# Kernel tuning notes

Hardware: AMD Instinct MI355X
Metric: run time of the kernel (lower is better)

The kernel has to match this reference:

```python
import jax
import jax.numpy as jnp
import numpy as np

# Periodic-boundary copy indices on the padded 18x18 lattice (dst <- src).
# None of the sources is an earlier destination, so one batched gather/scatter is faithful.
DST_R = np.array([1,1,2,3,4,4,6,7,8,10,11,12,14,14,15,16,17,17,16,15,14,14,12,10,8,6,4,4,3,2])
DST_C = np.array([3,5,7,9,10,11,13,13,14,15,15,16,15,16,15,14,13,11,9,7,6,5,3,2,1,0,0,1,1,2])
SRC_R = np.array([13,13,14,15,16,16,6,7,8,10,11,12,2,2,3,4,5,5,4,3,2,2,12,10,8,6,16,16,15,14])
SRC_C = np.array([15,5,7,9,10,11,1,1,2,3,3,4,3,4,3,2,1,11,9,7,6,5,15,14,13,12,12,13,13,14])

# 4x4 kernel sparsity masks (5 taps each)
_UP = np.zeros((4,4), np.float32);    _UP[[0,0,1,2,2],[0,1,1,1,2]] = 1
_LEFT = np.zeros((4,4), np.float32);  _LEFT[[1,2,2,2,3],[1,0,1,2,1]] = 1
_RIGHT = np.zeros((4,4), np.float32); _RIGHT[[1,2,2,2,3],[1,1,2,3,3]] = 1

def _out_mask():
    m = np.ones((16,16), np.float32)
    for i in range(9):
        m[i, 7+i:16] = 0
    for i in range(7):
        m[9+i, 0:i+1] = 0
    m[0,4:7]=0; m[1,6:8]=0; m[2,8]=0; m[3,9]=0
    m[6,12]=0; m[7,13]=0; m[8,14]=0; m[9,14]=0; m[10,14]=0; m[11,15]=0
    m[13:,14:]=0; m[15,13]=0; m[15,7:9]=0; m[13,5]=0; m[14,6]=0
    m[8,0]=0; m[9,1]=0; m[7,0]=0; m[3,0]=0; m[0:3,0:2]=0; m[0,2]=0
    return m
OUT_MASK = _out_mask()

def _conv(x, w, b):
    # kernel 4, stride 2, no padding: [B,C,18,18] -> [B,O,8,8]
    y = jax.lax.conv_general_dilated(x, w, window_strides=(2,2), padding='VALID',
                                     dimension_numbers=('NCHW','OIHW','NCHW'))
    return y + b[None, :, None, None]

def setup_inputs() -> dict:
    key = jax.random.key(0)
    ks = jax.random.split(key, 7)
    B, C, O = 2048, 64, 64
    x = jax.random.normal(ks[0], (B, C, 16, 16), dtype=jnp.float32)
    w_up = jax.random.normal(ks[1], (O, C, 4, 4), dtype=jnp.float32) * 0.05
    b_up = jax.random.normal(ks[2], (O,), dtype=jnp.float32) * 0.05
    w_left = jax.random.normal(ks[3], (O, C, 4, 4), dtype=jnp.float32) * 0.05
    b_left = jax.random.normal(ks[4], (O,), dtype=jnp.float32) * 0.05
    w_right = jax.random.normal(ks[5], (O, C, 4, 4), dtype=jnp.float32) * 0.05
    b_right = jax.random.normal(ks[6], (O,), dtype=jnp.float32) * 0.05
    return {"x": x, "w_up": w_up, "b_up": b_up, "w_left": w_left,
            "b_left": b_left, "w_right": w_right, "b_right": b_right}

def reference(x, w_up, b_up, w_left, b_left, w_right, b_right):
    # 1) zero-pad to 18x18 and apply periodic-boundary indexed copies
    xp = jnp.pad(x, ((0,0),(0,0),(1,1),(1,1)))
    xp = xp.at[:, :, DST_R, DST_C].set(xp[:, :, SRC_R, SRC_C])
    # 2) masked directional convs [B,O,8,8]
    up = _conv(xp, w_up * jnp.asarray(_UP), b_up)
    left = _conv(xp, w_left * jnp.asarray(_LEFT), b_left)
    right = _conv(xp, w_right * jnp.asarray(_RIGHT), b_right)
    # 3) interleave into 16x16: even rows = (up | 0) interleaved cols,
    #    odd rows = (left | right) interleaved cols
    B, O = up.shape[0], up.shape[1]
    out = jnp.zeros((B, O, 16, 16), x.dtype)
    out = out.at[:, :, 0::2, 0::2].set(up)
    out = out.at[:, :, 1::2, 0::2].set(left)
    out = out.at[:, :, 1::2, 1::2].set(right)
    # 4) static zero-out of non-lattice sites
    return out * jnp.asarray(OUT_MASK)
```

## Files before the change

### kernel.cpp

```cpp
#include <hip/hip_runtime.h>
#include <stdint.h>
#include <stddef.h>

typedef __attribute__((ext_vector_type(4))) float    f32x4;
typedef __attribute__((ext_vector_type(2))) float    f32x2;
typedef __attribute__((ext_vector_type(4))) uint32_t u32x4;
typedef __attribute__((ext_vector_type(8))) __bf16   bf16x8;

#define CGS   5200
#define NFRAG 15360

__device__ __constant__ uint8_t TAPR[15] = {0,0,1,2,2, 1,2,2,2,3, 1,2,2,2,3};
__device__ __constant__ uint8_t TAPC[15] = {0,1,1,1,2, 1,0,1,2,1, 1,1,2,3,3};

__device__ __constant__ uint8_t PDR[30] = {1,1,2,3,4,4,6,7,8,10,11,12,14,14,15,16,17,17,16,15,14,14,12,10,8,6,4,4,3,2};
__device__ __constant__ uint8_t PDC[30] = {3,5,7,9,10,11,13,13,14,15,15,16,15,16,15,14,13,11,9,7,6,5,3,2,1,0,0,1,1,2};
__device__ __constant__ uint8_t PSR[30] = {13,13,14,15,16,16,6,7,8,10,11,12,2,2,3,4,5,5,4,3,2,2,12,10,8,6,16,16,15,14};
__device__ __constant__ uint8_t PSC[30] = {15,5,7,9,10,11,1,1,2,3,3,4,3,4,3,2,1,11,9,7,6,5,15,14,13,12,12,13,13,14};

__device__ __forceinline__ uint32_t pk2(float a, float b) {
    return (uint32_t)__builtin_bit_cast(uint16_t, (__bf16)a)
         | ((uint32_t)__builtin_bit_cast(uint16_t, (__bf16)b) << 16);
}

__global__ __launch_bounds__(256) void pack_w(const float* __restrict__ wu,
                                              const float* __restrict__ wl,
                                              const float* __restrict__ wr,
                                              uint16_t* __restrict__ pw) {
    int fid = blockIdx.x * 256 + threadIdx.x;
    if (fid >= NFRAG) return;
    int lane = fid & 63;
    int mt   = (fid >> 6) & 3;
    int kk   = (fid >> 8) & 1;
    int td   = fid >> 9;
    const float* w = (td < 5) ? wu : (td < 10) ? wl : wr;
    int o  = mt * 16 + (lane & 15);
    int cb = kk * 32 + (lane >> 4) * 8;
    int kr = TAPR[td], kc = TAPC[td];
    const float* src = w + ((size_t)o * 64 + cb) * 16 + kr * 4 + kc;
    uint32_t d[4];
#pragma unroll
    for (int p = 0; p < 4; ++p)
        d[p] = pk2(src[(2 * p) * 16], src[(2 * p + 1) * 16]);
    u32x4 v = {d[0], d[1], d[2], d[3]};
    *(u32x4*)(pw + (size_t)fid * 8) = v;
}

__device__ __forceinline__ int slotof(int r, int c) { return (c & 1) * 162 + r * 9 + (c >> 1); }

__global__ __launch_bounds__(256, 3) void kagome_main(const float* __restrict__ x,
                                                      const uint16_t* __restrict__ pw,
                                                      const float* __restrict__ bu,
                                                      const float* __restrict__ bl,
                                                      const float* __restrict__ br,
                                                      float* __restrict__ out) {
    __shared__ __align__(16) uint8_t lds[8 * CGS];
    const int tid = threadIdx.x;
    const int b   = blockIdx.x;

    {
        const float* xb = x + (size_t)b * 16384;
#pragma unroll
        for (int i = 0; i < 2; ++i) {
            const int t    = i * 256 + tid;
            const int cg   = t >> 6;
            const int quad = t & 63;
            const int r0   = quad >> 2;
            const int qc   = quad & 3;
            f32x4 v[8];
#pragma unroll
            for (int ch = 0; ch < 8; ++ch)
                v[ch] = *(const f32x4*)(xb + (cg * 8 + ch) * 256 + quad * 4);
            uint8_t* base = lds + cg * CGS;
#pragma unroll
            for (int e = 0; e < 4; ++e) {
                const int pc   = 4 * qc + e + 1;
                const int slot = slotof(r0 + 1, pc);
                u32x4 w = {pk2(v[0][e], v[1][e]), pk2(v[2][e], v[3][e]),
                           pk2(v[4][e], v[5][e]), pk2(v[6][e], v[7][e])};
                *(u32x4*)(base + slot * 16) = w;
            }
        }
        u32x4 z = {0, 0, 0, 0};
        for (int idx = tid; idx < 68 * 8; idx += 256) {
            int s = idx >> 3, cg = idx & 7;
            int r, c;
            if (s < 18)      { r = 0;  c = s; }
            else if (s < 36) { r = 17; c = s - 18; }
            else             { int k2 = s - 36; r = 1 + (k2 >> 1); c = (k2 & 1) * 17; }
            *(u32x4*)(lds + cg * CGS + slotof(r, c) * 16) = z;
        }
    }
    __syncthreads();
    if (tid < 240) {
        int pair = tid >> 3, cg = tid & 7;
        int sa = slotof(PSR[pair], PSC[pair]);
        int da = slotof(PDR[pair], PDC[pair]);
        u32x4 v = *(const u32x4*)(lds + cg * CGS + sa * 16);
        *(u32x4*)(lds + cg * CGS + da * 16) = v;
    }
    __syncthreads();

    const int l   = tid & 63;
    const int wid = tid >> 6;
    const int q   = l >> 4;
    const int io  = (l >> 3) & 1;
    const int j   = l & 7;

    f32x4 acc[3][4];
#pragma unroll
    for (int d2 = 0; d2 < 3; ++d2)
#pragma unroll
        for (int n2 = 0; n2 < 4; ++n2) acc[d2][n2] = (f32x4){0.f, 0.f, 0.f, 0.f};

    const int bbase = q * CGS + io * 288 + j * 16;
    const uint16_t* pwl = pw + (size_t)l * 8;

#pragma unroll
    for (int kk = 0; kk < 2; ++kk) {
        bf16x8 aw[15];
#pragma unroll
        for (int f2 = 0; f2 < 15; ++f2) {
            u32x4 t = *(const u32x4*)(pwl + (size_t)((f2 * 2 + kk) * 4 + wid) * 512);
            aw[f2] = __builtin_bit_cast(bf16x8, t);
        }
        const uint8_t* lb = lds + kk * (4 * CGS) + bbase;
#pragma unroll
        for (int nt = 0; nt < 4; ++nt) {
#define BRD(dr, dc) __builtin_bit_cast(bf16x8, *(const u32x4*)(lb + ((dc) & 1) * 2592 + (4 * nt + (dr)) * 144 + ((dc) >> 1) * 16))
            bf16x8 b00 = BRD(0, 0);
            acc[0][nt] = __builtin_amdgcn_mfma_f32_16x16x32_bf16(aw[0], b00, acc[0][nt], 0, 0, 0);
            bf16x8 b01 = BRD(0, 1);
            acc[0][nt] = __builtin_amdgcn_mfma_f32_16x16x32_bf16(aw[1], b01, acc[0][nt], 0, 0, 0);
            bf16x8 b11 = BRD(1, 1);
            acc[0][nt] = __builtin_amdgcn_mfma_f32_16x16x32_bf16(aw[2],  b11, acc[0][nt], 0, 0, 0);
            acc[1][nt] = __builtin_amdgcn_mfma_f32_16x16x32_bf16(aw[5],  b11, acc[1][nt], 0, 0, 0);
            acc[2][nt] = __builtin_amdgcn_mfma_f32_16x16x32_bf16(aw[10], b11, acc[2][nt], 0, 0, 0);
            bf16x8 b20 = BRD(2, 0);
            acc[1][nt] = __builtin_amdgcn_mfma_f32_16x16x32_bf16(aw[6],  b20, acc[1][nt], 0, 0, 0);
            bf16x8 b21 = BRD(2, 1);
            acc[0][nt] = __builtin_amdgcn_mfma_f32_16x16x32_bf16(aw[3],  b21, acc[0][nt], 0, 0, 0);
            acc[1][nt] = __builtin_amdgcn_mfma_f32_16x16x32_bf16(aw[7],  b21, acc[1][nt], 0, 0, 0);
            acc[2][nt] = __builtin_amdgcn_mfma_f32_16x16x32_bf16(aw[11], b21, acc[2][nt], 0, 0, 0);
            bf16x8 b22 = BRD(2, 2);
            acc[0][nt] = __builtin_amdgcn_mfma_f32_16x16x32_bf16(aw[4],  b22, acc[0][nt], 0, 0, 0);
            acc[1][nt] = __builtin_amdgcn_mfma_f32_16x16x32_bf16(aw[8],  b22, acc[1][nt], 0, 0, 0);
            acc[2][nt] = __builtin_amdgcn_mfma_f32_16x16x32_bf16(aw[12], b22, acc[2][nt], 0, 0, 0);
            bf16x8 b23 = BRD(2, 3);
            acc[2][nt] = __builtin_amdgcn_mfma_f32_16x16x32_bf16(aw[13], b23, acc[2][nt], 0, 0, 0);
            bf16x8 b31 = BRD(3, 1);
            acc[1][nt] = __builtin_amdgcn_mfma_f32_16x16x32_bf16(aw[9],  b31, acc[1][nt], 0, 0, 0);
            bf16x8 b33 = BRD(3, 3);
            acc[2][nt] = __builtin_amdgcn_mfma_f32_16x16x32_bf16(aw[14], b33, acc[2][nt], 0, 0, 0);
#undef BRD
        }
    }

    float bias0[4], bias1[4], bias2[4];
#pragma unroll
    for (int r = 0; r < 4; ++r) {
        int o = wid * 16 + q * 4 + r;
        bias0[r] = bu[o]; bias1[r] = bl[o]; bias2[r] = br[o];
    }

    constexpr uint32_t RM[16] = {0x0008, 0x003C, 0x00FC, 0x01FE, 0x07FF, 0x0FFF, 0x0FFF, 0x1FFE,
                                 0x3FFE, 0xBFFC, 0xBFFC, 0x7FF8, 0xFFF0, 0x3FC0, 0x3F80, 0x1E00};
#pragma unroll
    for (int nt = 0; nt < 4; ++nt) {
        const int row_e = 4 * nt + 2 * io;
        const uint32_t me = io ? RM[4 * nt + 2] : RM[4 * nt + 0];
        const uint32_t mo = io ? RM[4 * nt + 3] : RM[4 * nt + 1];
        const uint32_t be  = (me >> (2 * j)) & 1u;
        const uint32_t bo0 = (mo >> (2 * j)) & 1u;
        const uint32_t bo1 = (mo >> (2 * j + 1)) & 1u;
#pragma unroll
        for (int r = 0; r < 4; ++r) {
            int o = wid * 16 + q * 4 + r;
            float up = acc[0][nt][r] + bias0[r];
            float lf = acc[1][nt][r] + bias1[r];
            float rt = acc[2][nt][r] + bias2[r];
            up = be  ? up : 0.f;
            lf = bo0 ? lf : 0.f;
            rt = bo1 ? rt : 0.f;
            float* po = out + (((size_t)b * 64 + o) * 256 + row_e * 16 + 2 * j);
            *(f32x2*)po        = (f32x2){up, 0.f};
            *(f32x2*)(po + 16) = (f32x2){lf, rt};
        }
    }
}

extern "C" void kernel_launch(void* const* d_in, const int* in_sizes, int n_in,
                              void* d_out, int out_size, void* d_ws, size_t ws_size,
                              hipStream_t stream) {
    const float* x  = (const float*)d_in[0];
    const float* wu = (const float*)d_in[1];
    const float* bu = (const float*)d_in[2];
    const float* wl = (const float*)d_in[3];
    const float* bl = (const float*)d_in[4];
    const float* wr = (const float*)d_in[5];
    const float* br = (const float*)d_in[6];
    float* out   = (float*)d_out;
    uint16_t* pw = (uint16_t*)d_ws;

    int B = in_sizes[0] / 16384;
    pack_w<<<(NFRAG + 255) / 256, 256, 0, stream>>>(wu, wl, wr, pw);
    kagome_main<<<B, 256, 0, stream>>>(x, pw, bu, bl, br, out);
}
```

Measured before the change: 62.44 us.

## Split each image's N tiles across 8 waves with 512-thread blocks

Doubles the block to 512 threads so each wave computes two of the four spatial N-tiles instead of all four, halving per-wave accumulators and MFMA work. The input staging loop collapses to one iteration per thread. The aim is more latency hiding and shorter per-block critical paths. In exchange, each wave pair reloads the same A-fragment weights from global memory, doubling weight traffic, and the launch-bounds occupancy target of 6 may constrain register allocation.

After: 86.78 us. +39.0%, slower.

```diff
diff --git a/kernel.cpp b/kernel.cpp
--- a/kernel.cpp
+++ b/kernel.cpp
@@ -48,7 +48,7 @@
 
 __device__ __forceinline__ int slotof(int r, int c) { return (c & 1) * 162 + r * 9 + (c >> 1); }
 
-__global__ __launch_bounds__(256, 3) void kagome_main(const float* __restrict__ x,
+__global__ __launch_bounds__(512, 6) void kagome_main(const float* __restrict__ x,
                                                       const uint16_t* __restrict__ pw,
                                                       const float* __restrict__ bu,
                                                       const float* __restrict__ bl,
@@ -60,35 +60,31 @@
 
     {
         const float* xb = x + (size_t)b * 16384;
-#pragma unroll
-        for (int i = 0; i < 2; ++i) {
-            const int t    = i * 256 + tid;
-            const int cg   = t >> 6;
-            const int quad = t & 63;
-            const int r0   = quad >> 2;
-            const int qc   = quad & 3;
-            f32x4 v[8];
-#pragma unroll
-            for (int ch = 0; ch < 8; ++ch)
-                v[ch] = *(const f32x4*)(xb + (cg * 8 + ch) * 256 + quad * 4);
-            uint8_t* base = lds + cg * CGS;
-#pragma unroll
-            for (int e = 0; e < 4; ++e) {
-                const int pc   = 4 * qc + e + 1;
-                const int slot = slotof(r0 + 1, pc);
-                u32x4 w = {pk2(v[0][e], v[1][e]), pk2(v[2][e], v[3][e]),
-                           pk2(v[4][e], v[5][e]), pk2(v[6][e], v[7][e])};
-                *(u32x4*)(base + slot * 16) = w;
-            }
+        const int cg   = tid >> 6;
+        const int quad = tid & 63;
+        const int r0   = quad >> 2;
+        const int qc   = quad & 3;
+        f32x4 v[8];
+#pragma unroll
+        for (int ch = 0; ch < 8; ++ch)
+            v[ch] = *(const f32x4*)(xb + (cg * 8 + ch) * 256 + quad * 4);
+        uint8_t* base = lds + cg * CGS;
+#pragma unroll
+        for (int e = 0; e < 4; ++e) {
+            const int pc   = 4 * qc + e + 1;
+            const int slot = slotof(r0 + 1, pc);
+            u32x4 w = {pk2(v[0][e], v[1][e]), pk2(v[2][e], v[3][e]),
+                       pk2(v[4][e], v[5][e]), pk2(v[6][e], v[7][e])};
+            *(u32x4*)(base + slot * 16) = w;
         }
         u32x4 z = {0, 0, 0, 0};
-        for (int idx = tid; idx < 68 * 8; idx += 256) {
-            int s = idx >> 3, cg = idx & 7;
+        for (int idx = tid; idx < 68 * 8; idx += 512) {
+            int s = idx >> 3, cg2 = idx & 7;
             int r, c;
             if (s < 18)      { r = 0;  c = s; }
             else if (s < 36) { r = 17; c = s - 18; }
             else             { int k2 = s - 36; r = 1 + (k2 >> 1); c = (k2 & 1) * 17; }
-            *(u32x4*)(lds + cg * CGS + slotof(r, c) * 16) = z;
+            *(u32x4*)(lds + cg2 * CGS + slotof(r, c) * 16) = z;
         }
     }
     __syncthreads();
@@ -103,15 +99,17 @@
 
     const int l   = tid & 63;
     const int wid = tid >> 6;
+    const int wm  = wid & 3;
+    const int ws  = wid >> 2;
     const int q   = l >> 4;
     const int io  = (l >> 3) & 1;
     const int j   = l & 7;
 
-    f32x4 acc[3][4];
+    f32x4 acc[3][2];
 #pragma unroll
     for (int d2 = 0; d2 < 3; ++d2)
 #pragma unroll
-        for (int n2 = 0; n2 < 4; ++n2) acc[d2][n2] = (f32x4){0.f, 0.f, 0.f, 0.f};
+        for (int n2 = 0; n2 < 2; ++n2) acc[d2][n2] = (f32x4){0.f, 0.f, 0.f, 0.f};
 
     const int bbase = q * CGS + io * 288 + j * 16;
     const uint16_t* pwl = pw + (size_t)l * 8;
@@ -121,37 +119,38 @@
         bf16x8 aw[15];
 #pragma unroll
         for (int f2 = 0; f2 < 15; ++f2) {
-            u32x4 t = *(const u32x4*)(pwl + (size_t)((f2 * 2 + kk) * 4 + wid) * 512);
+            u32x4 t = *(const u32x4*)(pwl + (size_t)((f2 * 2 + kk) * 4 + wm) * 512);
             aw[f2] = __builtin_bit_cast(bf16x8, t);
         }
         const uint8_t* lb = lds + kk * (4 * CGS) + bbase;
 #pragma unroll
-        for (int nt = 0; nt < 4; ++nt) {
+        for (int n2 = 0; n2 < 2; ++n2) {
+            const int nt = ws * 2 + n2;
 #define BRD(dr, dc) __builtin_bit_cast(bf16x8, *(const u32x4*)(lb + ((dc) & 1) * 2592 + (4 * nt + (dr)) * 144 + ((dc) >> 1) * 16))
             bf16x8 b00 = BRD(0, 0);
-            acc[0][nt] = __builtin_amdgcn_mfma_f32_16x16x32_bf16(aw[0], b00, acc[0][nt], 0, 0, 0);
+            acc[0][n2] = __builtin_amdgcn_mfma_f32_16x16x32_bf16(aw[0], b00, acc[0][n2], 0, 0, 0);
             bf16x8 b01 = BRD(0, 1);
-            acc[0][nt] = __builtin_amdgcn_mfma_f32_16x16x32_bf16(aw[1], b01, acc[0][nt], 0, 0, 0);
+            acc[0][n2] = __builtin_amdgcn_mfma_f32_16x16x32_bf16(aw[1], b01, acc[0][n2], 0, 0, 0);
             bf16x8 b11 = BRD(1, 1);
-            acc[0][nt] = __builtin_amdgcn_mfma_f32_16x16x32_bf16(aw[2],  b11, acc[0][nt], 0, 0, 0);
-            acc[1][nt] = __builtin_amdgcn_mfma_f32_16x16x32_bf16(aw[5],  b11, acc[1][nt], 0, 0, 0);
-            acc[2][nt] = __builtin_amdgcn_mfma_f32_16x16x32_bf16(aw[10], b11, acc[2][nt], 0, 0, 0);
+            acc[0][n2] = __builtin_amdgcn_mfma_f32_16x16x32_bf16(aw[2],  b11, acc[0][n2], 0, 0, 0);
+            acc[1][n2] = __builtin_amdgcn_mfma_f32_16x16x32_bf16(aw[5],  b11, acc[1][n2], 0, 0, 0);
+            acc[2][n2] = __builtin_amdgcn_mfma_f32_16x16x32_bf16(aw[10], b11, acc[2][n2], 0, 0, 0);
             bf16x8 b20 = BRD(2, 0);
-            acc[1][nt] = __builtin_amdgcn_mfma_f32_16x16x32_bf16(aw[6],  b20, acc[1][nt], 0, 0, 0);
+            acc[1][n2] = __builtin_amdgcn_mfma_f32_16x16x32_bf16(aw[6],  b20, acc[1][n2], 0, 0, 0);
             bf16x8 b21 = BRD(2, 1);
-            acc[0][nt] = __builtin_amdgcn_mfma_f32_16x16x32_bf16(aw[3],  b21, acc[0][nt], 0, 0, 0);
-            acc[1][nt] = __builtin_amdgcn_mfma_f32_16x16x32_bf16(aw[7],  b21, acc[1][nt], 0, 0, 0);
-            acc[2][nt] = __builtin_amdgcn_mfma_f32_16x16x32_bf16(aw[11], b21, acc[2][nt], 0, 0, 0);
+            acc[0][n2] = __builtin_amdgcn_mfma_f32_16x16x32_bf16(aw[3],  b21, acc[0][n2], 0, 0, 0);
+            acc[1][n2] = __builtin_amdgcn_mfma_f32_16x16x32_bf16(aw[7],  b21, acc[1][n2], 0, 0, 0);
+            acc[2][n2] = __builtin_amdgcn_mfma_f32_16x16x32_bf16(aw[11], b21, acc[2][n2], 0, 0, 0);
             bf16x8 b22 = BRD(2, 2);
-            acc[0][nt] = __builtin_amdgcn_mfma_f32_16x16x32_bf16(aw[4],  b22, acc[0][nt], 0, 0, 0);
-            acc[1][nt] = __builtin_amdgcn_mfma_f32_16x16x32_bf16(aw[8],  b22, acc[1][nt], 0, 0, 0);
-            acc[2][nt] = __builtin_amdgcn_mfma_f32_16x16x32_bf16(aw[12], b22, acc[2][nt], 0, 0, 0);
+            acc[0][n2] = __builtin_amdgcn_mfma_f32_16x16x32_bf16(aw[4],  b22, acc[0][n2], 0, 0, 0);
+            acc[1][n2] = __builtin_amdgcn_mfma_f32_16x16x32_bf16(aw[8],  b22, acc[1][n2], 0, 0, 0);
+            acc[2][n2] = __builtin_amdgcn_mfma_f32_16x16x32_bf16(aw[12], b22, acc[2][n2], 0, 0, 0);
             bf16x8 b23 = BRD(2, 3);
-            acc[2][nt] = __builtin_amdgcn_mfma_f32_16x16x32_bf16(aw[13], b23, acc[2][nt], 0, 0, 0);
+            acc[2][n2] = __builtin_amdgcn_mfma_f32_16x16x32_bf16(aw[13], b23, acc[2][n2], 0, 0, 0);
             bf16x8 b31 = BRD(3, 1);
-            acc[1][nt] = __builtin_amdgcn_mfma_f32_16x16x32_bf16(aw[9],  b31, acc[1][nt], 0, 0, 0);
+            acc[1][n2] = __builtin_amdgcn_mfma_f32_16x16x32_bf16(aw[9],  b31, acc[1][n2], 0, 0, 0);
             bf16x8 b33 = BRD(3, 3);
-            acc[2][nt] = __builtin_amdgcn_mfma_f32_16x16x32_bf16(aw[14], b33, acc[2][nt], 0, 0, 0);
+            acc[2][n2] = __builtin_amdgcn_mfma_f32_16x16x32_bf16(aw[14], b33, acc[2][n2], 0, 0, 0);
 #undef BRD
         }
     }
@@ -159,14 +158,15 @@
     float bias0[4], bias1[4], bias2[4];
 #pragma unroll
     for (int r = 0; r < 4; ++r) {
-        int o = wid * 16 + q * 4 + r;
+        int o = wm * 16 + q * 4 + r;
         bias0[r] = bu[o]; bias1[r] = bl[o]; bias2[r] = br[o];
     }
 
     constexpr uint32_t RM[16] = {0x0008, 0x003C, 0x00FC, 0x01FE, 0x07FF, 0x0FFF, 0x0FFF, 0x1FFE,
                                  0x3FFE, 0xBFFC, 0xBFFC, 0x7FF8, 0xFFF0, 0x3FC0, 0x3F80, 0x1E00};
 #pragma unroll
-    for (int nt = 0; nt < 4; ++nt) {
+    for (int n2 = 0; n2 < 2; ++n2) {
+        const int nt = ws * 2 + n2;
         const int row_e = 4 * nt + 2 * io;
         const uint32_t me = io ? RM[4 * nt + 2] : RM[4 * nt + 0];
         const uint32_t mo = io ? RM[4 * nt + 3] : RM[4 * nt + 1];
@@ -175,10 +175,10 @@
         const uint32_t bo1 = (mo >> (2 * j + 1)) & 1u;
 #pragma unroll
         for (int r = 0; r < 4; ++r) {
-            int o = wid * 16 + q * 4 + r;
-            float up = acc[0][nt][r] + bias0[r];
-            float lf = acc[1][nt][r] + bias1[r];
-            float rt = acc[2][nt][r] + bias2[r];
+            int o = wm * 16 + q * 4 + r;
+            float up = acc[0][n2][r] + bias0[r];
+            float lf = acc[1][n2][r] + bias1[r];
+            float rt = acc[2][n2][r] + bias2[r];
             up = be  ? up : 0.f;
             lf = bo0 ? lf : 0.f;
             rt = bo1 ? rt : 0.f;
@@ -204,5 +204,5 @@
 
     int B = in_sizes[0] / 16384;
     pack_w<<<(NFRAG + 255) / 256, 256, 0, stream>>>(wu, wl, wr, pw);
-    kagome_main<<<B, 256, 0, stream>>>(x, pw, bu, bl, br, out);
-}
+    kagome_main<<<B, 512, 0, stream>>>(x, pw, bu, bl, br, out);
+}
```

## Process four batch items per block with register prefetch of next input

Applied to the files above, without the earlier changes.

Each block now loops over four batch images instead of one, keeping boundary zeroing, bias and mask setup outside the loop. The next image's global loads are issued into registers before the MFMA phase of the current image, overlapping memory latency with compute. This costs more registers (launch bounds lowered from 3 to 2 blocks per CU), an extra barrier per iteration, and a grid four times smaller, which reduces parallelism. It also assumes B is divisible by four.

After: 92.30 us. +47.8%, slower.

```diff
diff --git a/kernel.cpp b/kernel.cpp
--- a/kernel.cpp
+++ b/kernel.cpp
@@ -9,6 +9,7 @@
 
 #define CGS   5200
 #define NFRAG 15360
+#define NB    4
 
 __device__ __constant__ uint8_t TAPR[15] = {0,0,1,2,2, 1,2,2,2,3, 1,2,2,2,3};
 __device__ __constant__ uint8_t TAPC[15] = {0,1,1,1,2, 1,0,1,2,1, 1,1,2,3,3};
@@ -48,7 +49,7 @@
 
 __device__ __forceinline__ int slotof(int r, int c) { return (c & 1) * 162 + r * 9 + (c >> 1); }
 
-__global__ __launch_bounds__(256, 3) void kagome_main(const float* __restrict__ x,
+__global__ __launch_bounds__(256, 2) void kagome_main(const float* __restrict__ x,
                                                       const uint16_t* __restrict__ pw,
                                                       const float* __restrict__ bu,
                                                       const float* __restrict__ bl,
@@ -56,105 +57,21 @@
                                                       float* __restrict__ out) {
     __shared__ __align__(16) uint8_t lds[8 * CGS];
     const int tid = threadIdx.x;
-    const int b   = blockIdx.x;
-
-    {
-        const float* xb = x + (size_t)b * 16384;
-#pragma unroll
-        for (int i = 0; i < 2; ++i) {
-            const int t    = i * 256 + tid;
-            const int cg   = t >> 6;
-            const int quad = t & 63;
-            const int r0   = quad >> 2;
-            const int qc   = quad & 3;
-            f32x4 v[8];
-#pragma unroll
-            for (int ch = 0; ch < 8; ++ch)
-                v[ch] = *(const f32x4*)(xb + (cg * 8 + ch) * 256 + quad * 4);
-            uint8_t* base = lds + cg * CGS;
-#pragma unroll
-            for (int e = 0; e < 4; ++e) {
-                const int pc   = 4 * qc + e + 1;
-                const int slot = slotof(r0 + 1, pc);
-                u32x4 w = {pk2(v[0][e], v[1][e]), pk2(v[2][e], v[3][e]),
-                           pk2(v[4][e], v[5][e]), pk2(v[6][e], v[7][e])};
-                *(u32x4*)(base + slot * 16) = w;
-            }
-        }
-        u32x4 z = {0, 0, 0, 0};
-        for (int idx = tid; idx < 68 * 8; idx += 256) {
-            int s = idx >> 3, cg = idx & 7;
-            int r, c;
-            if (s < 18)      { r = 0;  c = s; }
-            else if (s < 36) { r = 17; c = s - 18; }
-            else             { int k2 = s - 36; r = 1 + (k2 >> 1); c = (k2 & 1) * 17; }
-            *(u32x4*)(lds + cg * CGS + slotof(r, c) * 16) = z;
-        }
-    }
-    __syncthreads();
-    if (tid < 240) {
-        int pair = tid >> 3, cg = tid & 7;
-        int sa = slotof(PSR[pair], PSC[pair]);
-        int da = slotof(PDR[pair], PDC[pair]);
-        u32x4 v = *(const u32x4*)(lds + cg * CGS + sa * 16);
-        *(u32x4*)(lds + cg * CGS + da * 16) = v;
-    }
-    __syncthreads();
+    const int b0  = blockIdx.x * NB;
+
+    const int cgA  = tid >> 6;
+    const int cgB  = cgA + 4;
+    const int quad = tid & 63;
+    const int r0   = quad >> 2;
+    const int qc   = quad & 3;
 
     const int l   = tid & 63;
     const int wid = tid >> 6;
     const int q   = l >> 4;
     const int io  = (l >> 3) & 1;
     const int j   = l & 7;
-
-    f32x4 acc[3][4];
-#pragma unroll
-    for (int d2 = 0; d2 < 3; ++d2)
-#pragma unroll
-        for (int n2 = 0; n2 < 4; ++n2) acc[d2][n2] = (f32x4){0.f, 0.f, 0.f, 0.f};
-
     const int bbase = q * CGS + io * 288 + j * 16;
     const uint16_t* pwl = pw + (size_t)l * 8;
-
-#pragma unroll
-    for (int kk = 0; kk < 2; ++kk) {
-        bf16x8 aw[15];
-#pragma unroll
-        for (int f2 = 0; f2 < 15; ++f2) {
-            u32x4 t = *(const u32x4*)(pwl + (size_t)((f2 * 2 + kk) * 4 + wid) * 512);
-            aw[f2] = __builtin_bit_cast(bf16x8, t);
-        }
-        const uint8_t* lb = lds + kk * (4 * CGS) + bbase;
-#pragma unroll
-        for (int nt = 0; nt < 4; ++nt) {
-#define BRD(dr, dc) __builtin_bit_cast(bf16x8, *(const u32x4*)(lb + ((dc) & 1) * 2592 + (4 * nt + (dr)) * 144 + ((dc) >> 1) * 16))
-            bf16x8 b00 = BRD(0, 0);
-            acc[0][nt] = __builtin_amdgcn_mfma_f32_16x16x32_bf16(aw[0], b00, acc[0][nt], 0, 0, 0);
-            bf16x8 b01 = BRD(0, 1);
-            acc[0][nt] = __builtin_amdgcn_mfma_f32_16x16x32_bf16(aw[1], b01, acc[0][nt], 0, 0, 0);
-            bf16x8 b11 = BRD(1, 1);
-            acc[0][nt] = __builtin_amdgcn_mfma_f32_16x16x32_bf16(aw[2],  b11, acc[0][nt], 0, 0, 0);
-            acc[1][nt] = __builtin_amdgcn_mfma_f32_16x16x32_bf16(aw[5],  b11, acc[1][nt], 0, 0, 0);
-            acc[2][nt] = __builtin_amdgcn_mfma_f32_16x16x32_bf16(aw[10], b11, acc[2][nt], 0, 0, 0);
-            bf16x8 b20 = BRD(2, 0);
-            acc[1][nt] = __builtin_amdgcn_mfma_f32_16x16x32_bf16(aw[6],  b20, acc[1][nt], 0, 0, 0);
-            bf16x8 b21 = BRD(2, 1);
-            acc[0][nt] = __builtin_amdgcn_mfma_f32_16x16x32_bf16(aw[3],  b21, acc[0][nt], 0, 0, 0);
-            acc[1][nt] = __builtin_amdgcn_mfma_f32_16x16x32_bf16(aw[7],  b21, acc[1][nt], 0, 0, 0);
-            acc[2][nt] = __builtin_amdgcn_mfma_f32_16x16x32_bf16(aw[11], b21, acc[2][nt], 0, 0, 0);
-            bf16x8 b22 = BRD(2, 2);
-            acc[0][nt] = __builtin_amdgcn_mfma_f32_16x16x32_bf16(aw[4],  b22, acc[0][nt], 0, 0, 0);
-            acc[1][nt] = __builtin_amdgcn_mfma_f32_16x16x32_bf16(aw[8],  b22, acc[1][nt], 0, 0, 0);
-            acc[2][nt] = __builtin_amdgcn_mfma_f32_16x16x32_bf16(aw[12], b22, acc[2][nt], 0, 0, 0);
-            bf16x8 b23 = BRD(2, 3);
-            acc[2][nt] = __builtin_amdgcn_mfma_f32_16x16x32_bf16(aw[13], b23, acc[2][nt], 0, 0, 0);
-            bf16x8 b31 = BRD(3, 1);
-            acc[1][nt] = __builtin_amdgcn_mfma_f32_16x16x32_bf16(aw[9],  b31, acc[1][nt], 0, 0, 0);
-            bf16x8 b33 = BRD(3, 3);
-            acc[2][nt] = __builtin_amdgcn_mfma_f32_16x16x32_bf16(aw[14], b33, acc[2][nt], 0, 0, 0);
-#undef BRD
-        }
-    }
 
     float bias0[4], bias1[4], bias2[4];
 #pragma unroll
@@ -162,29 +79,135 @@
         int o = wid * 16 + q * 4 + r;
         bias0[r] = bu[o]; bias1[r] = bl[o]; bias2[r] = br[o];
     }
-
     constexpr uint32_t RM[16] = {0x0008, 0x003C, 0x00FC, 0x01FE, 0x07FF, 0x0FFF, 0x0FFF, 0x1FFE,
                                  0x3FFE, 0xBFFC, 0xBFFC, 0x7FF8, 0xFFF0, 0x3FC0, 0x3F80, 0x1E00};
+    uint32_t be[4], bo0[4], bo1[4];
 #pragma unroll
     for (int nt = 0; nt < 4; ++nt) {
-        const int row_e = 4 * nt + 2 * io;
         const uint32_t me = io ? RM[4 * nt + 2] : RM[4 * nt + 0];
         const uint32_t mo = io ? RM[4 * nt + 3] : RM[4 * nt + 1];
-        const uint32_t be  = (me >> (2 * j)) & 1u;
-        const uint32_t bo0 = (mo >> (2 * j)) & 1u;
-        const uint32_t bo1 = (mo >> (2 * j + 1)) & 1u;
-#pragma unroll
-        for (int r = 0; r < 4; ++r) {
-            int o = wid * 16 + q * 4 + r;
-            float up = acc[0][nt][r] + bias0[r];
-            float lf = acc[1][nt][r] + bias1[r];
-            float rt = acc[2][nt][r] + bias2[r];
-            up = be  ? up : 0.f;
-            lf = bo0 ? lf : 0.f;
-            rt = bo1 ? rt : 0.f;
-            float* po = out + (((size_t)b * 64 + o) * 256 + row_e * 16 + 2 * j);
-            *(f32x2*)po        = (f32x2){up, 0.f};
-            *(f32x2*)(po + 16) = (f32x2){lf, rt};
+        be[nt]  = (me >> (2 * j)) & 1u;
+        bo0[nt] = (mo >> (2 * j)) & 1u;
+        bo1[nt] = (mo >> (2 * j + 1)) & 1u;
+    }
+
+    {
+        u32x4 z = {0, 0, 0, 0};
+        for (int idx = tid; idx < 68 * 8; idx += 256) {
+            int s = idx >> 3, cg2 = idx & 7;
+            int r, c;
+            if (s < 18)      { r = 0;  c = s; }
+            else if (s < 36) { r = 17; c = s - 18; }
+            else             { int k2 = s - 36; r = 1 + (k2 >> 1); c = (k2 & 1) * 17; }
+            *(u32x4*)(lds + cg2 * CGS + slotof(r, c) * 16) = z;
+        }
+    }
+
+    f32x4 vA[8], vB[8];
+    {
+        const float* xb = x + (size_t)b0 * 16384 + quad * 4;
+#pragma unroll
+        for (int ch = 0; ch < 8; ++ch) {
+            vA[ch] = *(const f32x4*)(xb + (cgA * 8 + ch) * 256);
+            vB[ch] = *(const f32x4*)(xb + (cgB * 8 + ch) * 256);
+        }
+    }
+
+    for (int it = 0; it < NB; ++it) {
+        {
+            uint8_t* baseA = lds + cgA * CGS;
+            uint8_t* baseB = lds + cgB * CGS;
+#pragma unroll
+            for (int e = 0; e < 4; ++e) {
+                const int slot = slotof(r0 + 1, 4 * qc + e + 1);
+                u32x4 wa = {pk2(vA[0][e], vA[1][e]), pk2(vA[2][e], vA[3][e]),
+                            pk2(vA[4][e], vA[5][e]), pk2(vA[6][e], vA[7][e])};
+                u32x4 wb = {pk2(vB[0][e], vB[1][e]), pk2(vB[2][e], vB[3][e]),
+                            pk2(vB[4][e], vB[5][e]), pk2(vB[6][e], vB[7][e])};
+                *(u32x4*)(baseA + slot * 16) = wa;
+                *(u32x4*)(baseB + slot * 16) = wb;
+            }
+        }
+        __syncthreads();
+        if (tid < 240) {
+            int pair = tid >> 3, cg = tid & 7;
+            u32x4 v = *(const u32x4*)(lds + cg * CGS + slotof(PSR[pair], PSC[pair]) * 16);
+            *(u32x4*)(lds + cg * CGS + slotof(PDR[pair], PDC[pair]) * 16) = v;
+        }
+        if (it < NB - 1) {
+            const float* xb = x + (size_t)(b0 + it + 1) * 16384 + quad * 4;
+#pragma unroll
+            for (int ch = 0; ch < 8; ++ch) {
+                vA[ch] = *(const f32x4*)(xb + (cgA * 8 + ch) * 256);
+                vB[ch] = *(const f32x4*)(xb + (cgB * 8 + ch) * 256);
+            }
+        }
+        __syncthreads();
+
+        f32x4 acc[3][4];
+#pragma unroll
+        for (int d2 = 0; d2 < 3; ++d2)
+#pragma unroll
+            for (int n2 = 0; n2 < 4; ++n2) acc[d2][n2] = (f32x4){0.f, 0.f, 0.f, 0.f};
+
+#pragma unroll
+        for (int kk = 0; kk < 2; ++kk) {
+            bf16x8 aw[15];
+#pragma unroll
+            for (int f2 = 0; f2 < 15; ++f2) {
+                u32x4 t = *(const u32x4*)(pwl + (size_t)((f2 * 2 + kk) * 4 + wid) * 512);
+                aw[f2] = __builtin_bit_cast(bf16x8, t);
+            }
+            const uint8_t* lb = lds + kk * (4 * CGS) + bbase;
+#pragma unroll
+            for (int nt = 0; nt < 4; ++nt) {
+#define BRD(dr, dc) __builtin_bit_cast(bf16x8, *(const u32x4*)(lb + ((dc) & 1) * 2592 + (4 * nt + (dr)) * 144 + ((dc) >> 1) * 16))
+                bf16x8 b00 = BRD(0, 0);
+                acc[0][nt] = __builtin_amdgcn_mfma_f32_16x16x32_bf16(aw[0], b00, acc[0][nt], 0, 0, 0);
+                bf16x8 b01 = BRD(0, 1);
+                acc[0][nt] = __builtin_amdgcn_mfma_f32_16x16x32_bf16(aw[1], b01, acc[0][nt], 0, 0, 0);
+                bf16x8 b11 = BRD(1, 1);
+                acc[0][nt] = __builtin_amdgcn_mfma_f32_16x16x32_bf16(aw[2],  b11, acc[0][nt], 0, 0, 0);
+                acc[1][nt] = __builtin_amdgcn_mfma_f32_16x16x32_bf16(aw[5],  b11, acc[1][nt], 0, 0, 0);
+                acc[2][nt] = __builtin_amdgcn_mfma_f32_16x16x32_bf16(aw[10], b11, acc[2][nt], 0, 0, 0);
+                bf16x8 b20 = BRD(2, 0);
+                acc[1][nt] = __builtin_amdgcn_mfma_f32_16x16x32_bf16(aw[6],  b20, acc[1][nt], 0, 0, 0);
+                bf16x8 b21 = BRD(2, 1);
+                acc[0][nt] = __builtin_amdgcn_mfma_f32_16x16x32_bf16(aw[3],  b21, acc[0][nt], 0, 0, 0);
+                acc[1][nt] = __builtin_amdgcn_mfma_f32_16x16x32_bf16(aw[7],  b21, acc[1][nt], 0, 0, 0);
+                acc[2][nt] = __builtin_amdgcn_mfma_f32_16x16x32_bf16(aw[11], b21, acc[2][nt], 0, 0, 0);
+                bf16x8 b22 = BRD(2, 2);
+                acc[0][nt] = __builtin_amdgcn_mfma_f32_16x16x32_bf16(aw[4],  b22, acc[0][nt], 0, 0, 0);
+                acc[1][nt] = __builtin_amdgcn_mfma_f32_16x16x32_bf16(aw[8],  b22, acc[1][nt], 0, 0, 0);
+                acc[2][nt] = __builtin_amdgcn_mfma_f32_16x16x32_bf16(aw[12], b22, acc[2][nt], 0, 0, 0);
+                bf16x8 b23 = BRD(2, 3);
+                acc[2][nt] = __builtin_amdgcn_mfma_f32_16x16x32_bf16(aw[13], b23, acc[2][nt], 0, 0, 0);
+                bf16x8 b31 = BRD(3, 1);
+                acc[1][nt] = __builtin_amdgcn_mfma_f32_16x16x32_bf16(aw[9],  b31, acc[1][nt], 0, 0, 0);
+                bf16x8 b33 = BRD(3, 3);
+                acc[2][nt] = __builtin_amdgcn_mfma_f32_16x16x32_bf16(aw[14], b33, acc[2][nt], 0, 0, 0);
+#undef BRD
+            }
+        }
+        __syncthreads();
+
+        const int b = b0 + it;
+#pragma unroll
+        for (int nt = 0; nt < 4; ++nt) {
+            const int row_e = 4 * nt + 2 * io;
+#pragma unroll
+            for (int r = 0; r < 4; ++r) {
+                int o = wid * 16 + q * 4 + r;
+                float up = acc[0][nt][r] + bias0[r];
+                float lf = acc[1][nt][r] + bias1[r];
+                float rt = acc[2][nt][r] + bias2[r];
+                up = be[nt]  ? up : 0.f;
+                lf = bo0[nt] ? lf : 0.f;
+                rt = bo1[nt] ? rt : 0.f;
+                float* po = out + (((size_t)b * 64 + o) * 256 + row_e * 16 + 2 * j);
+                *(f32x2*)po        = (f32x2){up, 0.f};
+                *(f32x2*)(po + 16) = (f32x2){lf, rt};
+            }
         }
     }
 }
@@ -204,5 +227,5 @@
 
     int B = in_sizes[0] / 16384;
     pack_w<<<(NFRAG + 255) / 256, 256, 0, stream>>>(wu, wl, wr, pw);
-    kagome_main<<<B, 256, 0, stream>>>(x, pw, bu, bl, br, out);
-}
+    kagome_main<<<B / NB, 256, 0, stream>>>(x, pw, bu, bl, br, out);
+}
```
